# Kernel optimization log

Measured on AMD Instinct MI355X. Metric: run time of the kernel, lower is better.

The kernel has to match this reference:

```python
import jax, jax.numpy as jnp
import numpy as np

NUM_NODES = 50000
HIDDEN = 128
NUM_REL = 8
NUM_EDGES = 600000


def setup_inputs() -> dict:
    key = jax.random.key(0)
    ks = jax.random.split(key, 10)
    s = 1.0 / np.sqrt(HIDDEN)
    return {
        "edge_index": jax.random.randint(ks[0], (2, NUM_EDGES), 0, NUM_NODES, dtype=jnp.int32),
        "edge_type": jax.random.randint(ks[1], (NUM_EDGES,), 0, NUM_REL, dtype=jnp.int32),
        "node_emb": jax.random.normal(ks[2], (NUM_NODES, HIDDEN), jnp.float32),
        "W1": jax.random.normal(ks[3], (NUM_REL, HIDDEN, HIDDEN), jnp.float32) * s,
        "root1": jax.random.normal(ks[4], (HIDDEN, HIDDEN), jnp.float32) * s,
        "b1": jnp.zeros((HIDDEN,), jnp.float32),
        "W2": jax.random.normal(ks[5], (NUM_REL, HIDDEN, HIDDEN), jnp.float32) * s,
        "root2": jax.random.normal(ks[6], (HIDDEN, HIDDEN), jnp.float32) * s,
        "b2": jnp.zeros((HIDDEN,), jnp.float32),
    }


def rgcn_layer(x, W, root, bias, src, dst, rel):
    # PyG RGCNConv: per-relation MEAN aggregation of neighbor features,
    # transformed by relation weight, plus root transform and bias.
    N = x.shape[0]
    R = W.shape[0]
    # transform node features by every relation weight: [N, R, F]
    xw = jnp.einsum('nd,rdf->nrf', x, W)
    # per-(dst, relation) in-edge counts for mean normalization
    cnt = jnp.zeros((N, R), x.dtype).at[dst, rel].add(1.0)
    inv = 1.0 / jnp.maximum(cnt, 1.0)
    # per-edge message, normalized by destination's per-relation degree
    msg = xw[src, rel] * inv[dst, rel][:, None]  # [E, F]
    agg = jnp.zeros((N, W.shape[2]), x.dtype).at[dst].add(msg)
    return agg + x @ root + bias


def reference(edge_index, edge_type, node_emb, W1, root1, b1, W2, root2, b2):
    src, dst = edge_index[0], edge_index[1]
    h = jax.nn.relu(rgcn_layer(node_emb, W1, root1, b1, src, dst, edge_type))
    out = rgcn_layer(h, W2, root2, b2, src, dst, edge_type)
    return out
```

## Files before the change

kernel.cpp:

```cpp
#include <hip/hip_runtime.h>

#define H 128
#define RREL 8
#define NJ 9
#define CURPAD 16

typedef short bf16x8 __attribute__((ext_vector_type(8)));
typedef float f32x4 __attribute__((ext_vector_type(4)));
typedef unsigned short u16x8 __attribute__((ext_vector_type(8)));

static __device__ __forceinline__ unsigned short f2bf(float f) {
    unsigned int u = __float_as_uint(f);
    unsigned int r = (u + 0x7fffu + ((u >> 16) & 1u)) >> 16;
    return (unsigned short)r;
}
static __device__ __forceinline__ float bf2f(unsigned short u) {
    return __uint_as_float(((unsigned int)u) << 16);
}

__global__ void zero_kernel(int* p, long n) {
    long i = (long)blockIdx.x * blockDim.x + threadIdx.x;
    long stride = (long)gridDim.x * blockDim.x;
    for (; i < n; i += stride) p[i] = 0;
}

__global__ void count_kernel(const int* __restrict__ ei, const int* __restrict__ et,
                             int* __restrict__ cnt, int E) {
    int e = blockIdx.x * 256 + threadIdx.x;
    if (e >= E) return;
    int d = ei[E + e];
    int r = et[e];
    atomicAdd(&cnt[(size_t)d * RREL + r], 1);
}

__global__ void scan_block_kernel(const int* __restrict__ cnt, int* __restrict__ rploc,
                                  int* __restrict__ bsum, int N) {
    __shared__ int s[256];
    int t = threadIdx.x;
    int d = blockIdx.x * 256 + t;
    int v = 0;
    if (d < N) {
#pragma unroll
        for (int r = 0; r < RREL; ++r) v += cnt[(size_t)d * RREL + r];
    }
    s[t] = v;
    __syncthreads();
#pragma unroll
    for (int off = 1; off < 256; off <<= 1) {
        int u = 0;
        if (t >= off) u = s[t - off];
        __syncthreads();
        s[t] += u;
        __syncthreads();
    }
    if (d < N) rploc[d] = s[t] - v;
    if (t == 255) bsum[blockIdx.x] = s[255];
}

__global__ void scan_top_kernel(const int* __restrict__ bsum, int* __restrict__ boff, int nb) {
    __shared__ int s[256];
    int t = threadIdx.x;
    int v = (t < nb) ? bsum[t] : 0;
    s[t] = v;
    __syncthreads();
#pragma unroll
    for (int off = 1; off < 256; off <<= 1) {
        int u = 0;
        if (t >= off) u = s[t - off];
        __syncthreads();
        s[t] += u;
        __syncthreads();
    }
    boff[t] = s[t] - v;
}

__global__ void finalize_kernel(const int* __restrict__ cnt, const int* __restrict__ rploc,
                                const int* __restrict__ boff, int* __restrict__ rowptr,
                                float* __restrict__ inv, int N) {
    int d = blockIdx.x * 256 + threadIdx.x;
    if (d >= N) return;
    int rp = rploc[d] + boff[d >> 8];
    rowptr[d] = rp;
    int deg = 0;
#pragma unroll
    for (int r = 0; r < RREL; ++r) {
        int c = cnt[(size_t)d * RREL + r];
        inv[(size_t)d * RREL + r] = 1.0f / (float)max(c, 1);
        deg += c;
    }
    if (d == N - 1) rowptr[N] = rp + deg;
}

__global__ void fill_kernel(const int* __restrict__ ei, const int* __restrict__ et,
                            int* __restrict__ cursor_pad, const int* __restrict__ rowptr,
                            int* __restrict__ packed, int E) {
    int e = blockIdx.x * 256 + threadIdx.x;
    if (e >= E) return;
    int d = ei[E + e];
    int pos = rowptr[d] + atomicAdd(&cursor_pad[(size_t)d << 4], 1);
    packed[pos] = ei[e] | (et[e] << 20);
}

__global__ void tobf_kernel(const float* __restrict__ x, unsigned short* __restrict__ xb, long n) {
    long i = (long)blockIdx.x * blockDim.x + threadIdx.x;
    long stride = (long)gridDim.x * blockDim.x;
    for (; i < n; i += stride) xb[i] = f2bf(x[i]);
}

__global__ void wcat_kernel(const float* __restrict__ W1, const float* __restrict__ r1,
                            const float* __restrict__ W2, const float* __restrict__ r2,
                            const float* __restrict__ b1, const float* __restrict__ b2,
                            unsigned short* __restrict__ WTa1, unsigned short* __restrict__ WTa2,
                            float* __restrict__ biasP) {
    int id = blockIdx.x * 256 + threadIdx.x;
    const int per = NJ * H * H;
    if (id < per) {
        int j = id / (H * H);
        int fk = id - j * (H * H);
        int f = fk >> 7, k = fk & 127;
        float v = (j < RREL) ? W1[((size_t)j * H + k) * H + f] : r1[(size_t)k * H + f];
        WTa1[id] = f2bf(v);
        int ko = (k & 7) * 16 + (k >> 3);
        float v2 = (j < RREL) ? W2[((size_t)j * H + ko) * H + f] : r2[(size_t)ko * H + f];
        WTa2[id] = f2bf(v2);
    } else if (id < per + 2 * H) {
        int c = id - per;
        int cp = c & 127;
        int co = (cp & 7) * 16 + (cp >> 3);
        biasP[c] = (c < H) ? b1[co] : b2[co];
    }
}

__global__ __launch_bounds__(256) void xw_kernel(const unsigned short* __restrict__ xin,
                                                 const unsigned short* __restrict__ WTa,
                                                 unsigned short* __restrict__ Y,
                                                 int N, int j0, int j1) {
    __shared__ unsigned short Ws[128][136];
    const int t = threadIdx.x;
    const int w = t >> 6, l = t & 63;
    const int m_base = blockIdx.x * 128;
    const int colb = l & 15, quad = l >> 4;
    const f32x4 fz = {0.f, 0.f, 0.f, 0.f};

    int row0 = m_base + w * 32 + colb;
    int row1 = row0 + 16;
    const unsigned short* xr0 = xin + (size_t)(row0 < N ? row0 : N - 1) * H;
    const unsigned short* xr1 = xin + (size_t)(row1 < N ? row1 : N - 1) * H;

    for (int j = j0; j < j1; ++j) {
        __syncthreads();
#pragma unroll
        for (int p = 0; p < 8; ++p) {
            int c = p * 256 + t;
            int f = c >> 4, k8 = (c & 15) * 8;
            *(u16x8*)&Ws[f][k8] = *(const u16x8*)&WTa[((size_t)j * H + f) * H + k8];
        }
        __syncthreads();
        f32x4 acc[2][8];
#pragma unroll
        for (int mi = 0; mi < 2; ++mi)
#pragma unroll
            for (int n = 0; n < 8; ++n) acc[mi][n] = fz;
#pragma unroll
        for (int ks = 0; ks < 4; ++ks) {
            int kl = ks * 32 + quad * 8;
            bf16x8 a0 = *(const bf16x8*)&xr0[kl];
            bf16x8 a1 = *(const bf16x8*)&xr1[kl];
#pragma unroll
            for (int n = 0; n < 8; ++n) {
                bf16x8 b = *(const bf16x8*)&Ws[n * 16 + colb][kl];
                acc[0][n] = __builtin_amdgcn_mfma_f32_16x16x32_bf16(a0, b, acc[0][n], 0, 0, 0);
                acc[1][n] = __builtin_amdgcn_mfma_f32_16x16x32_bf16(a1, b, acc[1][n], 0, 0, 0);
            }
        }
        unsigned short* Yj = Y + (size_t)(j - j0) * N * H;
#pragma unroll
        for (int mi = 0; mi < 2; ++mi) {
#pragma unroll
            for (int i = 0; i < 4; ++i) {
                int row = m_base + w * 32 + mi * 16 + quad * 4 + i;
                if (row < N) {
                    u16x8 o;
#pragma unroll
                    for (int n = 0; n < 8; ++n) o[n] = f2bf(acc[mi][n][i]);
                    *(u16x8*)&Yj[(size_t)row * H + colb * 8] = o;
                }
            }
        }
    }
}

__global__ __launch_bounds__(256) void gather_kernel(const unsigned short* __restrict__ Y,
                                                     const float* __restrict__ inv,
                                                     const int* __restrict__ rowptr,
                                                     const int* __restrict__ packed,
                                                     const float* __restrict__ biasP,
                                                     float* __restrict__ accf,
                                                     float* __restrict__ outf,
                                                     unsigned short* __restrict__ outb,
                                                     int N, int relu, int j0, int j1, int final_pass) {
    const int t = threadIdx.x;
    const int l = t & 63;
    int d = blockIdx.x * 16 + (t >> 4);
    if (d >= N) return;
    const int fl = l & 15;
    const int kc = fl * 8;
    const int gbase = l & 48;
    int rp = 0;
    if (fl < 2) rp = rowptr[d + fl];
    float ivl = 0.f;
    if (fl < 8) ivl = inv[(size_t)d * RREL + fl];
    int beg = __shfl(rp, gbase);
    int end = __shfl(rp, gbase + 1);
    const int jr = (j1 < RREL) ? j1 : RREL;
    float tot[8] = {};
    for (int i = beg; i < end; i += 16) {
        int pk = (i + fl < end) ? packed[i + fl] : -1;
#pragma unroll
        for (int e = 0; e < 16; e += 4) {
            int v0 = __shfl(pk, gbase + e);
            int v1 = __shfl(pk, gbase + e + 1);
            int v2 = __shfl(pk, gbase + e + 2);
            int v3 = __shfl(pk, gbase + e + 3);
            int s0 = v0 & 0xFFFFF, r0 = v0 >> 20;
            int s1 = v1 & 0xFFFFF, r1 = v1 >> 20;
            int s2 = v2 & 0xFFFFF, r2 = v2 >> 20;
            int s3 = v3 & 0xFFFFF, r3 = v3 >> 20;
            if (r0 >= j0 && r0 < jr) {
                float iv = __shfl(ivl, gbase + r0);
                u16x8 v = *(const u16x8*)&Y[((size_t)(r0 - j0) * N + s0) * H + kc];
#pragma unroll
                for (int j = 0; j < 8; ++j) tot[j] += iv * bf2f((unsigned short)v[j]);
            }
            if (r1 >= j0 && r1 < jr) {
                float iv = __shfl(ivl, gbase + r1);
                u16x8 v = *(const u16x8*)&Y[((size_t)(r1 - j0) * N + s1) * H + kc];
#pragma unroll
                for (int j = 0; j < 8; ++j) tot[j] += iv * bf2f((unsigned short)v[j]);
            }
            if (r2 >= j0 && r2 < jr) {
                float iv = __shfl(ivl, gbase + r2);
                u16x8 v = *(const u16x8*)&Y[((size_t)(r2 - j0) * N + s2) * H + kc];
#pragma unroll
                for (int j = 0; j < 8; ++j) tot[j] += iv * bf2f((unsigned short)v[j]);
            }
            if (r3 >= j0 && r3 < jr) {
                float iv = __shfl(ivl, gbase + r3);
                u16x8 v = *(const u16x8*)&Y[((size_t)(r3 - j0) * N + s3) * H + kc];
#pragma unroll
                for (int j = 0; j < 8; ++j) tot[j] += iv * bf2f((unsigned short)v[j]);
            }
        }
    }
    if (j1 == NJ) {
        u16x8 vr = *(const u16x8*)&Y[((size_t)(RREL - j0) * N + d) * H + kc];
#pragma unroll
        for (int j = 0; j < 8; ++j) tot[j] += bf2f((unsigned short)vr[j]);
    }
    if (j0 > 0) {
        f32x4 p0 = *(const f32x4*)&accf[(size_t)d * H + kc];
        f32x4 p1 = *(const f32x4*)&accf[(size_t)d * H + kc + 4];
#pragma unroll
        for (int j = 0; j < 4; ++j) { tot[j] += p0[j]; tot[4 + j] += p1[j]; }
    }
    if (final_pass) {
        f32x4 b0 = *(const f32x4*)&biasP[kc];
        f32x4 b1 = *(const f32x4*)&biasP[kc + 4];
#pragma unroll
        for (int j = 0; j < 4; ++j) { tot[j] += b0[j]; tot[4 + j] += b1[j]; }
        if (relu) {
#pragma unroll
            for (int j = 0; j < 8; ++j) tot[j] = fmaxf(tot[j], 0.f);
        }
        if (outf) {
#pragma unroll
            for (int j = 0; j < 8; ++j) outf[(size_t)d * H + j * 16 + fl] = tot[j];
        } else {
            u16x8 o;
#pragma unroll
            for (int j = 0; j < 8; ++j) o[j] = f2bf(tot[j]);
            *(u16x8*)&outb[(size_t)d * H + kc] = o;
        }
    } else {
        f32x4 o0, o1;
#pragma unroll
        for (int j = 0; j < 4; ++j) { o0[j] = tot[j]; o1[j] = tot[4 + j]; }
        *(f32x4*)&accf[(size_t)d * H + kc] = o0;
        *(f32x4*)&accf[(size_t)d * H + kc + 4] = o1;
    }
}

extern "C" void kernel_launch(void* const* d_in, const int* in_sizes, int n_in,
                              void* d_out, int out_size, void* d_ws, size_t ws_size,
                              hipStream_t stream) {
    const int* edge_index = (const int*)d_in[0];
    const int* edge_type  = (const int*)d_in[1];
    const float* node_emb = (const float*)d_in[2];
    const float* W1    = (const float*)d_in[3];
    const float* root1 = (const float*)d_in[4];
    const float* b1    = (const float*)d_in[5];
    const float* W2    = (const float*)d_in[6];
    const float* root2 = (const float*)d_in[7];
    const float* b2    = (const float*)d_in[8];
    float* out = (float*)d_out;

    const int E = in_sizes[1];
    const int N = in_sizes[2] / H;

    char* base = (char*)d_ws;
    size_t off = 0;
    auto take = [&](size_t bytes) { size_t o = off; off = (off + bytes + 63) & ~(size_t)63; return o; };
    int*   cnt        = (int*)  (base + take((size_t)N * RREL * 4));
    int*   cursor_pad = (int*)  (base + take((size_t)N * CURPAD * 4));
    int*   rploc      = (int*)  (base + take((size_t)N * 4));
    int*   bsum       = (int*)  (base + take(256 * 4));
    int*   boff       = (int*)  (base + take(256 * 4));
    int*   rowptr     = (int*)  (base + take(((size_t)N + 1) * 4));
    float* inv        = (float*)(base + take((size_t)N * RREL * 4));
    int*   packed     = (int*)  (base + take((size_t)E * 4));
    unsigned short* WTa1 = (unsigned short*)(base + take((size_t)NJ * H * H * 2));
    unsigned short* WTa2 = (unsigned short*)(base + take((size_t)NJ * H * H * 2));
    float* biasP      = (float*)(base + take(2 * H * 4));
    unsigned short* xb = (unsigned short*)(base + take((size_t)N * H * 2));
    unsigned short* hb = (unsigned short*)(base + take((size_t)N * H * 2));

    size_t fixed_off = off;
    unsigned short* Y;
    float* accf = nullptr;
    int rc;
    size_t availA = (ws_size > fixed_off) ? ws_size - fixed_off : 0;
    if (availA >= (size_t)NJ * N * H * 2) {
        Y = (unsigned short*)(base + fixed_off);
        rc = NJ;
    } else {
        accf = (float*)(base + fixed_off);
        size_t off2 = fixed_off + (((size_t)N * H * 4 + 63) & ~(size_t)63);
        Y = (unsigned short*)(base + off2);
        size_t availB = (ws_size > off2) ? ws_size - off2 : 0;
        rc = (int)(availB / ((size_t)N * H * 2));
        if (rc > RREL) rc = RREL;
        if (rc < 1) rc = 1;
    }

    const int nbScan = (N + 255) / 256;

    zero_kernel<<<1024, 256, 0, stream>>>(cnt, (long)N * (RREL + CURPAD));
    count_kernel<<<(E + 255) / 256, 256, 0, stream>>>(edge_index, edge_type, cnt, E);
    scan_block_kernel<<<nbScan, 256, 0, stream>>>(cnt, rploc, bsum, N);
    scan_top_kernel<<<1, 256, 0, stream>>>(bsum, boff, nbScan);
    finalize_kernel<<<nbScan, 256, 0, stream>>>(cnt, rploc, boff, rowptr, inv, N);
    fill_kernel<<<(E + 255) / 256, 256, 0, stream>>>(edge_index, edge_type, cursor_pad, rowptr, packed, E);
    wcat_kernel<<<(NJ * H * H + 2 * H + 255) / 256, 256, 0, stream>>>(W1, root1, W2, root2, b1, b2,
                                                                      WTa1, WTa2, biasP);
    tobf_kernel<<<1024, 256, 0, stream>>>(node_emb, xb, (long)N * H);

    const int gx = (N + 127) / 128;
    const int gg = (N + 15) / 16;

    auto run_layer = [&](const unsigned short* xin, const unsigned short* WTa, const float* bp,
                         float* of, unsigned short* ob, int relu) {
        for (int j0 = 0; j0 < NJ; j0 += rc) {
            int j1 = (j0 + rc < NJ) ? j0 + rc : NJ;
            int fin = (j1 == NJ);
            xw_kernel<<<gx, 256, 0, stream>>>(xin, WTa, Y, N, j0, j1);
            gather_kernel<<<gg, 256, 0, stream>>>(Y, inv, rowptr, packed, bp, accf,
                                                  fin ? of : nullptr, fin ? ob : nullptr,
                                                  N, relu, j0, j1, fin);
        }
    };

    run_layer(xb, WTa1, biasP, nullptr, hb, 1);
    run_layer(hb, WTa2, biasP + H, out, nullptr, 0);
}
```

Measured before the change: 300.5 us.

## Split each destination's edges across four 16-lane groups with wave reduction

The gather kernel now assigns one wavefront per destination node instead of one 16-lane group per node. The four 16-lane groups each process every fourth edge, and the partial sums are combined with xor-shuffles. Edge metadata for the first 64 edges is loaded once per wave. Off-relation edges become branchless predicated loads of row 0 with zero weight, replacing divergent branches. This aims to raise memory-level parallelism for the random Y row reads, at the cost of 4x more blocks, cross-lane reductions, three idle groups during the epilogue, and wasted loads for edges filtered out by the relation chunk.

```diff
diff --git a/kernel.cpp b/kernel.cpp
--- a/kernel.cpp
+++ b/kernel.cpp
@@ -200,58 +200,59 @@
                                                      unsigned short* __restrict__ outb,
                                                      int N, int relu, int j0, int j1, int final_pass) {
     const int t = threadIdx.x;
-    const int l = t & 63;
-    int d = blockIdx.x * 16 + (t >> 4);
+    const int w = t >> 6, l = t & 63;
+    int d = blockIdx.x * 4 + w;
     if (d >= N) return;
-    const int fl = l & 15;
+    const int g = l >> 4, fl = l & 15;
     const int kc = fl * 8;
-    const int gbase = l & 48;
-    int rp = 0;
-    if (fl < 2) rp = rowptr[d + fl];
-    float ivl = 0.f;
-    if (fl < 8) ivl = inv[(size_t)d * RREL + fl];
-    int beg = __shfl(rp, gbase);
-    int end = __shfl(rp, gbase + 1);
+    const int gb = l & 48;
+    int beg = rowptr[d], end = rowptr[d + 1];
+    float ivl = (fl < 8) ? inv[(size_t)d * RREL + fl] : 0.f;
+    int pkb = (beg + l < end) ? packed[beg + l] : -1;
+    const int cnt = end - beg;
     const int jr = (j1 < RREL) ? j1 : RREL;
+    const int span = jr - j0;
     float tot[8] = {};
-    for (int i = beg; i < end; i += 16) {
-        int pk = (i + fl < end) ? packed[i + fl] : -1;
-#pragma unroll
-        for (int e = 0; e < 16; e += 4) {
-            int v0 = __shfl(pk, gbase + e);
-            int v1 = __shfl(pk, gbase + e + 1);
-            int v2 = __shfl(pk, gbase + e + 2);
-            int v3 = __shfl(pk, gbase + e + 3);
-            int s0 = v0 & 0xFFFFF, r0 = v0 >> 20;
-            int s1 = v1 & 0xFFFFF, r1 = v1 >> 20;
-            int s2 = v2 & 0xFFFFF, r2 = v2 >> 20;
-            int s3 = v3 & 0xFFFFF, r3 = v3 >> 20;
-            if (r0 >= j0 && r0 < jr) {
-                float iv = __shfl(ivl, gbase + r0);
-                u16x8 v = *(const u16x8*)&Y[((size_t)(r0 - j0) * N + s0) * H + kc];
-#pragma unroll
-                for (int j = 0; j < 8; ++j) tot[j] += iv * bf2f((unsigned short)v[j]);
-            }
-            if (r1 >= j0 && r1 < jr) {
-                float iv = __shfl(ivl, gbase + r1);
-                u16x8 v = *(const u16x8*)&Y[((size_t)(r1 - j0) * N + s1) * H + kc];
-#pragma unroll
-                for (int j = 0; j < 8; ++j) tot[j] += iv * bf2f((unsigned short)v[j]);
-            }
-            if (r2 >= j0 && r2 < jr) {
-                float iv = __shfl(ivl, gbase + r2);
-                u16x8 v = *(const u16x8*)&Y[((size_t)(r2 - j0) * N + s2) * H + kc];
-#pragma unroll
-                for (int j = 0; j < 8; ++j) tot[j] += iv * bf2f((unsigned short)v[j]);
-            }
-            if (r3 >= j0 && r3 < jr) {
-                float iv = __shfl(ivl, gbase + r3);
-                u16x8 v = *(const u16x8*)&Y[((size_t)(r3 - j0) * N + s3) * H + kc];
-#pragma unroll
-                for (int j = 0; j < 8; ++j) tot[j] += iv * bf2f((unsigned short)v[j]);
-            }
-        }
-    }
+    int lim = cnt < 64 ? cnt : 64;
+    int lim4 = (lim + 3) & ~3;
+    for (int idx = g; idx < lim4; idx += 4) {
+        int pk = __shfl(pkb, idx);
+        int s = pk & 0xFFFFF;
+        int r = pk >> 20;
+        int rr = r - j0;
+        bool ok = (unsigned)rr < (unsigned)span;
+        float iv = __shfl(ivl, gb + (r & 7));
+        iv = ok ? iv : 0.f;
+        int rowc = ok ? rr : 0;
+        int sc = ok ? s : 0;
+        u16x8 v = *(const u16x8*)&Y[((size_t)rowc * N + sc) * H + kc];
+#pragma unroll
+        for (int j = 0; j < 8; ++j) tot[j] += iv * bf2f((unsigned short)v[j]);
+    }
+    int tail_n = cnt - 64;
+    if (tail_n > 0) {
+        int tailN = (tail_n + 3) & ~3;
+        for (int o = g; o < tailN; o += 4) {
+            int pk = (o < tail_n) ? packed[beg + 64 + o] : -1;
+            int s = pk & 0xFFFFF;
+            int r = pk >> 20;
+            int rr = r - j0;
+            bool ok = (unsigned)rr < (unsigned)span;
+            float iv = __shfl(ivl, gb + (r & 7));
+            iv = ok ? iv : 0.f;
+            int rowc = ok ? rr : 0;
+            int sc = ok ? s : 0;
+            u16x8 v = *(const u16x8*)&Y[((size_t)rowc * N + sc) * H + kc];
+#pragma unroll
+            for (int j = 0; j < 8; ++j) tot[j] += iv * bf2f((unsigned short)v[j]);
+        }
+    }
+#pragma unroll
+    for (int j = 0; j < 8; ++j) {
+        tot[j] += __shfl_xor(tot[j], 16);
+        tot[j] += __shfl_xor(tot[j], 32);
+    }
+    if (g != 0) return;
     if (j1 == NJ) {
         u16x8 vr = *(const u16x8*)&Y[((size_t)(RREL - j0) * N + d) * H + kc];
 #pragma unroll
@@ -355,7 +356,7 @@
     tobf_kernel<<<1024, 256, 0, stream>>>(node_emb, xb, (long)N * H);
 
     const int gx = (N + 127) / 128;
-    const int gg = (N + 15) / 16;
+    const int gg = (N + 3) / 4;
 
     auto run_layer = [&](const unsigned short* xin, const unsigned short* WTa, const float* bp,
                          float* of, unsigned short* ob, int relu) {
```

Measured after the change: 297.9 us. No clear change (-0.9%).
